# Kernel tuning notes

Hardware: AMD Instinct MI355X
Metric: run time of the kernel (lower is better)

Reference implementation:

```python
import jax, jax.numpy as jnp
import numpy as np

BSZ, SLEN, DIN = 4, 2048, 1024
EMB, HNO = 1024, 16
HSZ = EMB // HNO


def setup_inputs() -> dict:
    key = jax.random.key(0)
    ks = jax.random.split(key, 7)
    s = 1.0 / np.sqrt(DIN)
    return {
        "x": jax.random.normal(ks[0], (BSZ, SLEN, DIN), dtype=jnp.float32),
        "Wq": jax.random.uniform(ks[1], (EMB, DIN), jnp.float32, -s, s),
        "bq": jax.random.uniform(ks[2], (EMB,), jnp.float32, -s, s),
        "Wk": jax.random.uniform(ks[3], (EMB, DIN), jnp.float32, -s, s),
        "bk": jax.random.uniform(ks[4], (EMB,), jnp.float32, -s, s),
        "Wv": jax.random.uniform(ks[5], (EMB, DIN), jnp.float32, -s, s),
        "bv": jax.random.uniform(ks[6], (EMB,), jnp.float32, -s, s),
    }


def reference(x, Wq, bq, Wk, bk, Wv, bv):
    bsz, slen, _ = x.shape
    # QKV projections, split heads: [b, h, s, hd]
    def proj(W, b):
        y = jnp.einsum('bsd,ed->bse', x, W) + b
        return y.reshape(bsz, slen, HNO, HSZ).transpose(0, 2, 1, 3)
    q, k, v = proj(Wq, bq), proj(Wk, bk), proj(Wv, bv)
    # scaled causal attention scores [b, h, s, s]
    scores = jnp.einsum('bhqd,bhkd->bhqk', q, k) / jnp.sqrt(jnp.asarray(HSZ, x.dtype))
    causal = jnp.tril(jnp.ones((slen, slen), dtype=bool))
    scores = jnp.where(causal[None, None], scores, -jnp.inf)
    attn = jax.nn.softmax(scores, axis=-1)
    value = jnp.einsum('bhqk,bhkd->bhqd', attn, v)  # [b, h, s, hd]
    # faithful to source: swap (s, hd) THEN flatten to [b, s, emb]
    value = jnp.swapaxes(value, -2, -1).reshape(bsz, slen, -1)
    return value
```

## Files before the change

### kernel.cpp

```cpp
#include <hip/hip_runtime.h>


#define BSZ 4
#define SLEN 2048
#define DIN 1024
#define EMB 1024
#define HNO 16
#define HSZ 64

typedef unsigned short u16;
typedef __bf16 bf16x8_t __attribute__((ext_vector_type(8)));
typedef float f32x4_t __attribute__((ext_vector_type(4)));

__device__ __forceinline__ u16 f2bf(float f) {
    unsigned u = __float_as_uint(f);
    u += 0x7FFFu + ((u >> 16) & 1u);
    return (u16)(u >> 16);
}

__device__ __forceinline__ float exp2_fast(float x) {
    float r;
    asm("v_exp_f32 %0, %1" : "=v"(r) : "v"(x));
    return r;
}

__device__ __forceinline__ unsigned cvt_pk_bf16(float lo, float hi) {
    unsigned r;
    asm("v_cvt_pk_bf16_f32 %0, %1, %2" : "=v"(r) : "v"(lo), "v"(hi));
    return r;
}

__device__ __forceinline__ void gld16(void* lds, const void* g) {
    __builtin_amdgcn_global_load_lds(
        (const __attribute__((address_space(1))) void*)g,
        (__attribute__((address_space(3))) void*)lds, 16, 0, 0);
}

#define VMW0()                                                                 \
    do {                                                                       \
        asm volatile("s_waitcnt vmcnt(0)" ::: "memory");                       \
        __builtin_amdgcn_sched_barrier(0);                                     \
    } while (0)

#define LGKM0()                                                                \
    do {                                                                       \
        asm volatile("s_waitcnt lgkmcnt(0)" ::: "memory");                     \
        __builtin_amdgcn_sched_barrier(0);                                     \
    } while (0)

__global__ __launch_bounds__(256) void cvt_bf16_kernel(
    const float* __restrict__ x,  const float* __restrict__ wq,
    const float* __restrict__ wk, const float* __restrict__ wv,
    u16* __restrict__ xo, u16* __restrict__ wo)
{
    const int y = blockIdx.y;
    const float* src = (y == 0) ? x : (y == 1) ? wq : (y == 2) ? wk : wv;
    u16* dst = (y == 0) ? xo : wo + (size_t)(y - 1) * (EMB * DIN);
    const int n8 = (y == 0) ? (BSZ * SLEN * DIN / 8) : (EMB * DIN / 8);

    for (int i = blockIdx.x * 256 + threadIdx.x; i < n8; i += gridDim.x * 256) {
        float4 a = *reinterpret_cast<const float4*>(src + (size_t)i * 8);
        float4 b = *reinterpret_cast<const float4*>(src + (size_t)i * 8 + 4);
        union { u16 h[8]; uint4 u; } p;
        p.h[0] = f2bf(a.x); p.h[1] = f2bf(a.y); p.h[2] = f2bf(a.z); p.h[3] = f2bf(a.w);
        p.h[4] = f2bf(b.x); p.h[5] = f2bf(b.y); p.h[6] = f2bf(b.z); p.h[7] = f2bf(b.w);
        *reinterpret_cast<uint4*>(dst + (size_t)i * 8) = p.u;
    }
}

__global__ __launch_bounds__(256, 2) void qkv_gemm_kernel(
    const u16* __restrict__ xb, const u16* __restrict__ wb,
    const float* __restrict__ bq, const float* __restrict__ bk,
    const float* __restrict__ bv,
    u16* __restrict__ qkv, u16* __restrict__ vt)
{
    __shared__ __attribute__((aligned(16))) u16 SH[2 * 16384 + 8192];
    u16* Bs = SH + 2 * 16384;

    const int t    = threadIdx.x;
    const int wid  = t >> 6;
    const int lane = t & 63;
    const int g    = lane >> 4;
    const int r16  = lane & 15;
    const int wm   = wid >> 1, wn = wid & 1;

    const int wg  = blockIdx.x;
    const int xcd = wg & 7;
    const int j   = wg >> 3;
    const int jm  = j / 12;
    const int jn  = j - jm * 12;
    const int m0  = ((xcd & 3) * 8 + jm) * 256;
    const int n0g = ((xcd >> 2) * 12 + jn) * 128;

    const int rowoff = t >> 3;
    const int colswz = ((t & 7) ^ (rowoff & 7)) * 8;
    const u16* srcA = xb + (size_t)(m0 + rowoff) * DIN + colswz;
    const u16* srcB = wb + (size_t)(n0g + rowoff) * DIN + colswz;

    const int s0 = (g ^ (r16 & 7)) * 8;

    f32x4_t acc[8][4] = {};

#pragma unroll
    for (int u = 0; u < 8; ++u)
        gld16(SH + u * 2048 + t * 8, srcA + (size_t)u * 32 * DIN);
#pragma unroll
    for (int v = 0; v < 4; ++v)
        gld16(Bs + v * 2048 + t * 8, srcB + (size_t)v * 32 * DIN);
    VMW0();
    __builtin_amdgcn_s_barrier();

#pragma unroll 1
    for (int kt = 0; kt < 16; ++kt) {
        const bool nl = (kt != 15);
        const u16* Acur = SH + (kt & 1) * 16384;
        u16*       Aalt = SH + ((kt + 1) & 1) * 16384;

        if (nl) {
#pragma unroll
            for (int u = 0; u < 8; ++u)
                gld16(Aalt + u * 2048 + t * 8,
                      srcA + (size_t)u * 32 * DIN + (kt + 1) * 64);
        }

        bf16x8_t af[8], bf0[4], bf1[4];
#pragma unroll
        for (int i2 = 0; i2 < 8; ++i2)
            af[i2] = *reinterpret_cast<const bf16x8_t*>(
                Acur + (wm * 128 + i2 * 16 + r16) * 64 + s0);
#pragma unroll
        for (int j2 = 0; j2 < 4; ++j2) {
            bf0[j2] = *reinterpret_cast<const bf16x8_t*>(
                Bs + (wn * 64 + j2 * 16 + r16) * 64 + s0);
            bf1[j2] = *reinterpret_cast<const bf16x8_t*>(
                Bs + (wn * 64 + j2 * 16 + r16) * 64 + (s0 ^ 32));
        }

        __builtin_amdgcn_s_setprio(1);
#pragma unroll
        for (int i2 = 0; i2 < 8; ++i2)
#pragma unroll
            for (int j2 = 0; j2 < 4; ++j2)
                acc[i2][j2] = __builtin_amdgcn_mfma_f32_16x16x32_bf16(
                    af[i2], bf0[j2], acc[i2][j2], 0, 0, 0);
        __builtin_amdgcn_s_setprio(0);

#pragma unroll
        for (int i2 = 0; i2 < 8; ++i2)
            af[i2] = *reinterpret_cast<const bf16x8_t*>(
                Acur + (wm * 128 + i2 * 16 + r16) * 64 + (s0 ^ 32));

        LGKM0();
        __builtin_amdgcn_s_barrier();

        if (nl) {
#pragma unroll
            for (int v = 0; v < 4; ++v)
                gld16(Bs + v * 2048 + t * 8,
                      srcB + (size_t)v * 32 * DIN + (kt + 1) * 64);
        }

        __builtin_amdgcn_s_setprio(1);
#pragma unroll
        for (int i2 = 0; i2 < 8; ++i2)
#pragma unroll
            for (int j2 = 0; j2 < 4; ++j2)
                acc[i2][j2] = __builtin_amdgcn_mfma_f32_16x16x32_bf16(
                    af[i2], bf1[j2], acc[i2][j2], 0, 0, 0);
        __builtin_amdgcn_s_setprio(0);

        VMW0();
        __builtin_amdgcn_s_barrier();
    }

    const size_t per = (size_t)BSZ * HNO * SLEN * HSZ;
    const bool isV = (n0g >= 2 * 1024);
    u16* lout = SH;
    const int b  = m0 >> 11;
    const int sB = m0 & 2047;
    const int mat = n0g >> 10;

#pragma unroll
    for (int h = 0; h < 2; ++h) {
        __syncthreads();
        if (!isV) {
            if (wm == h) {
#pragma unroll
                for (int j2 = 0; j2 < 4; ++j2) {
                    const int el = wn * 64 + j2 * 16 + r16;
                    const int e  = (n0g + el) & 1023;
                    const float bval = (mat == 0) ? bq[e] : bk[e];
                    const float qsv  = (mat == 0) ? 0.125f * 1.44269504f : 1.0f;
#pragma unroll
                    for (int i2 = 0; i2 < 8; ++i2)
#pragma unroll
                        for (int r = 0; r < 4; ++r) {
                            int ml = i2 * 16 + g * 4 + r;
                            lout[ml * 136 + el] =
                                f2bf((acc[i2][j2][r] + bval) * qsv);
                        }
                }
            }
            __syncthreads();
#pragma unroll
            for (int it = 0; it < 8; ++it) {
                int cid = it * 256 + t;
                int row = cid >> 4;
                int cc  = cid & 15;
                int e   = (n0g + cc * 8) & 1023;
                int s   = sB + h * 128 + row;
                uint4 v = *reinterpret_cast<const uint4*>(&lout[row * 136 + cc * 8]);
                *reinterpret_cast<uint4*>(qkv + (size_t)mat * per +
                    ((((size_t)b * HNO) + (e >> 6)) * SLEN + s) * HSZ + (e & 63)) = v;
            }
        } else {
            if (wm == h) {
#pragma unroll
                for (int j2 = 0; j2 < 4; ++j2) {
                    const int el = wn * 64 + j2 * 16 + r16;
                    const int e  = (n0g + el) & 1023;
                    const float bval = bv[e];
#pragma unroll
                    for (int i2 = 0; i2 < 8; ++i2) {
                        uint2 pk;
                        pk.x = cvt_pk_bf16(acc[i2][j2][0] + bval,
                                           acc[i2][j2][1] + bval);
                        pk.y = cvt_pk_bf16(acc[i2][j2][2] + bval,
                                           acc[i2][j2][3] + bval);
                        *reinterpret_cast<uint2*>(
                            &lout[el * 136 + i2 * 16 + g * 4]) = pk;
                    }
                }
            }
            __syncthreads();
#pragma unroll
            for (int it = 0; it < 8; ++it) {
                int cid = it * 256 + t;
                int el  = cid >> 4;
                int sc  = cid & 15;
                int egl = n0g + el;
                int hh  = (egl >> 6) & 15;
                int d   = egl & 63;
                int s   = sB + h * 128 + sc * 8;
                uint4 v = *reinterpret_cast<const uint4*>(&lout[el * 136 + sc * 8]);
                *reinterpret_cast<uint4*>(vt +
                    (((size_t)(b * HNO + hh)) * HSZ + d) * SLEN + s) = v;
            }
        }
    }
}

__global__ __launch_bounds__(512, 6) void attn_kernel(
    const u16* __restrict__ qb, const u16* __restrict__ kb,
    const u16* __restrict__ vtg, float* __restrict__ out)
{
    __shared__ __attribute__((aligned(16))) u16 Ks[2][64][64];
    __shared__ __attribute__((aligned(16))) u16 Vt[2][64][64];
    __shared__ __attribute__((aligned(16))) u16 P2[8][16][72];

    const int t    = threadIdx.x;
    const int wid  = t >> 6;
    const int lane = t & 63;
    const int g    = lane >> 4;
    const int r16  = lane & 15;
    const int r8   = r16 & 7;

    const int w   = blockIdx.x;
    const int idx = w >> 3;
    const int bh  = (w & 7) * 8 + (idx & 7);
    const int qt  = 15 - (idx >> 3);
    const int q0  = qt * 128;
    const size_t base = (size_t)bh * (SLEN * HSZ);

    const int qi = q0 + wid * 16 + r16;
    bf16x8_t qf0 = *reinterpret_cast<const bf16x8_t*>(&qb[base + (size_t)qi * HSZ + g * 8]);
    bf16x8_t qf1 = *reinterpret_cast<const bf16x8_t*>(&qb[base + (size_t)qi * HSZ + 32 + g * 8]);

    const int srow = t >> 3;
    const int schk = ((t & 7) ^ (srow & 7)) * 8;
    const u16* ksrc = kb  + base + (size_t)srow * HSZ + schk;
    const u16* vsrc = vtg + base + (size_t)srow * SLEN + schk;
    const int ldst = wid * 8 * 64;

    f32x4_t o[4] = {};
    float lrow = 0.f;

    const int ntiles = 2 * qt + 2;
    const int qw0 = q0 + wid * 16;
    const int qmax_wave = qw0 + 15;

    gld16(&Ks[0][0][0] + ldst, ksrc);
    gld16(&Vt[0][0][0] + ldst, vsrc);
    VMW0();
    __builtin_amdgcn_s_barrier();

#pragma unroll 1
    for (int kt = 0; kt < ntiles; ++kt) {
        const int kv0  = kt * 64;
        const int bsel = kt & 1;
        if (kt + 1 < ntiles) {
            gld16(&Ks[bsel ^ 1][0][0] + ldst, ksrc + (size_t)(kv0 + 64) * HSZ);
            gld16(&Vt[bsel ^ 1][0][0] + ldst, vsrc + (kv0 + 64));
        }

        if (kv0 <= qmax_wave) {
            const u16* Kb = &Ks[bsel][0][0];
            const u16* Vb = &Vt[bsel][0][0];

            f32x4_t c_[4];
            __builtin_amdgcn_s_setprio(1);
#pragma unroll
            for (int m = 0; m < 4; ++m) {
                bf16x8_t a0 = *reinterpret_cast<const bf16x8_t*>(
                    Kb + (m * 16 + r16) * 64 + (g ^ r8) * 8);
                bf16x8_t a1 = *reinterpret_cast<const bf16x8_t*>(
                    Kb + (m * 16 + r16) * 64 + ((4 + g) ^ r8) * 8);
                f32x4_t cc = {};
                cc = __builtin_amdgcn_mfma_f32_16x16x32_bf16(a0, qf0, cc, 0, 0, 0);
                cc = __builtin_amdgcn_mfma_f32_16x16x32_bf16(a1, qf1, cc, 0, 0, 0);
                c_[m] = cc;
            }
            __builtin_amdgcn_s_setprio(0);

            float p[16];
            if (kv0 + 63 > qw0) {
#pragma unroll
                for (int m = 0; m < 4; ++m)
#pragma unroll
                    for (int r = 0; r < 4; ++r) {
                        int kj = kv0 + m * 16 + g * 4 + r;
                        float sv = (kj <= qi) ? c_[m][r] : -1e30f;
                        p[m * 4 + r] = exp2_fast(sv - 4.0f);
                    }
            } else {
#pragma unroll
                for (int m = 0; m < 4; ++m)
#pragma unroll
                    for (int r = 0; r < 4; ++r)
                        p[m * 4 + r] = exp2_fast(c_[m][r] - 4.0f);
            }
            float y0 = (p[0] + p[1]) + (p[2] + p[3]);
            float y1 = (p[4] + p[5]) + (p[6] + p[7]);
            float y2 = (p[8] + p[9]) + (p[10] + p[11]);
            float y3 = (p[12] + p[13]) + (p[14] + p[15]);
            float tsum = (y0 + y1) + (y2 + y3);
            tsum += __shfl_xor(tsum, 16);
            tsum += __shfl_xor(tsum, 32);
            lrow += tsum;

#pragma unroll
            for (int m = 0; m < 4; ++m) {
                uint2 pk;
                pk.x = cvt_pk_bf16(p[m * 4 + 0], p[m * 4 + 1]);
                pk.y = cvt_pk_bf16(p[m * 4 + 2], p[m * 4 + 3]);
                *reinterpret_cast<uint2*>(&P2[wid][r16][m * 16 + g * 4]) = pk;
            }

            __builtin_amdgcn_s_setprio(1);
#pragma unroll
            for (int c = 0; c < 2; ++c) {
                bf16x8_t pf = *reinterpret_cast<const bf16x8_t*>(
                    &P2[wid][r16][c * 32 + g * 8]);
#pragma unroll
                for (int j2 = 0; j2 < 4; ++j2) {
                    bf16x8_t vf = *reinterpret_cast<const bf16x8_t*>(
                        Vb + (j2 * 16 + r16) * 64 + ((c * 4 + g) ^ r8) * 8);
                    o[j2] = __builtin_amdgcn_mfma_f32_16x16x32_bf16(
                        vf, pf, o[j2], 0, 0, 0);
                }
            }
            __builtin_amdgcn_s_setprio(0);
        }

        VMW0();
        __builtin_amdgcn_s_barrier();
    }

    float rinv = 1.0f / lrow;
    const int b = bh >> 4, h = bh & 15;
    float* outb = out + (size_t)b * (SLEN * EMB) + (size_t)h * (HSZ * SLEN);
#pragma unroll
    for (int j2 = 0; j2 < 4; ++j2) {
#pragma unroll
        for (int r = 0; r < 4; ++r) {
            int d = j2 * 16 + g * 4 + r;
            outb[(size_t)d * SLEN + qi] = o[j2][r] * rinv;
        }
    }
}

extern "C" void kernel_launch(void* const* d_in, const int* in_sizes, int n_in,
                              void* d_out, int out_size, void* d_ws, size_t ws_size,
                              hipStream_t stream) {
    const float* x  = (const float*)d_in[0];
    const float* Wq = (const float*)d_in[1];
    const float* bq = (const float*)d_in[2];
    const float* Wk = (const float*)d_in[3];
    const float* bk = (const float*)d_in[4];
    const float* Wv = (const float*)d_in[5];
    const float* bv = (const float*)d_in[6];
    float* out = (float*)d_out;

    const size_t per = (size_t)BSZ * HNO * SLEN * HSZ;
    u16* qw = (u16*)d_ws;
    u16* kw = qw + per;
    u16* vw = kw + per;

    u16* xb = (u16*)d_out;
    u16* wb = xb + (size_t)BSZ * SLEN * DIN;

    cvt_bf16_kernel<<<dim3(256, 4), 256, 0, stream>>>(x, Wq, Wk, Wv, xb, wb);
    qkv_gemm_kernel<<<768, 256, 0, stream>>>(xb, wb, bq, bk, bv, qw, vw);
    attn_kernel<<<1024, 512, 0, stream>>>(qw, kw, vw, out);
}
```

Measured before the change: 122.2 us.

## Single-buffer A tile in QKV GEMM to shrink LDS and raise occupancy

Replaces the double-buffered A tile with one A buffer, cutting the GEMM's shared memory from about 80KB to 48KB. All next-tile global loads for A and B now issue after the second-half fragment reads and the barrier, and sched_barriers pin that ordering. The aim is lower LDS use, likely allowing more resident workgroups, and less register pressure from reusing one B fragment array. The cost is less overlap: the A prefetch no longer runs during the first half's MFMAs, so load latency is hidden only behind the second half.

```diff
diff --git a/kernel.cpp b/kernel.cpp
--- a/kernel.cpp
+++ b/kernel.cpp
@@ -74,8 +74,9 @@
     const float* __restrict__ bv,
     u16* __restrict__ qkv, u16* __restrict__ vt)
 {
-    __shared__ __attribute__((aligned(16))) u16 SH[2 * 16384 + 8192];
-    u16* Bs = SH + 2 * 16384;
+    __shared__ __attribute__((aligned(16))) u16 SH[256 * 64 + 128 * 64];
+    u16* AsF = SH;
+    u16* BsF = SH + 256 * 64;
 
     const int t    = threadIdx.x;
     const int wid  = t >> 6;
@@ -103,38 +104,25 @@
 
 #pragma unroll
     for (int u = 0; u < 8; ++u)
-        gld16(SH + u * 2048 + t * 8, srcA + (size_t)u * 32 * DIN);
+        gld16(AsF + u * 2048 + t * 8, srcA + (size_t)u * 32 * DIN);
 #pragma unroll
     for (int v = 0; v < 4; ++v)
-        gld16(Bs + v * 2048 + t * 8, srcB + (size_t)v * 32 * DIN);
+        gld16(BsF + v * 2048 + t * 8, srcB + (size_t)v * 32 * DIN);
     VMW0();
     __builtin_amdgcn_s_barrier();
 
 #pragma unroll 1
     for (int kt = 0; kt < 16; ++kt) {
-        const bool nl = (kt != 15);
-        const u16* Acur = SH + (kt & 1) * 16384;
-        u16*       Aalt = SH + ((kt + 1) & 1) * 16384;
-
-        if (nl) {
-#pragma unroll
-            for (int u = 0; u < 8; ++u)
-                gld16(Aalt + u * 2048 + t * 8,
-                      srcA + (size_t)u * 32 * DIN + (kt + 1) * 64);
-        }
-
-        bf16x8_t af[8], bf0[4], bf1[4];
+        bf16x8_t af[8], bf[4];
+
 #pragma unroll
         for (int i2 = 0; i2 < 8; ++i2)
             af[i2] = *reinterpret_cast<const bf16x8_t*>(
-                Acur + (wm * 128 + i2 * 16 + r16) * 64 + s0);
-#pragma unroll
-        for (int j2 = 0; j2 < 4; ++j2) {
-            bf0[j2] = *reinterpret_cast<const bf16x8_t*>(
-                Bs + (wn * 64 + j2 * 16 + r16) * 64 + s0);
-            bf1[j2] = *reinterpret_cast<const bf16x8_t*>(
-                Bs + (wn * 64 + j2 * 16 + r16) * 64 + (s0 ^ 32));
-        }
+                AsF + (wm * 128 + i2 * 16 + r16) * 64 + s0);
+#pragma unroll
+        for (int j2 = 0; j2 < 4; ++j2)
+            bf[j2] = *reinterpret_cast<const bf16x8_t*>(
+                BsF + (wn * 64 + j2 * 16 + r16) * 64 + s0);
 
         __builtin_amdgcn_s_setprio(1);
 #pragma unroll
@@ -142,23 +130,33 @@
 #pragma unroll
             for (int j2 = 0; j2 < 4; ++j2)
                 acc[i2][j2] = __builtin_amdgcn_mfma_f32_16x16x32_bf16(
-                    af[i2], bf0[j2], acc[i2][j2], 0, 0, 0);
+                    af[i2], bf[j2], acc[i2][j2], 0, 0, 0);
         __builtin_amdgcn_s_setprio(0);
 
 #pragma unroll
         for (int i2 = 0; i2 < 8; ++i2)
             af[i2] = *reinterpret_cast<const bf16x8_t*>(
-                Acur + (wm * 128 + i2 * 16 + r16) * 64 + (s0 ^ 32));
+                AsF + (wm * 128 + i2 * 16 + r16) * 64 + (s0 ^ 32));
+#pragma unroll
+        for (int j2 = 0; j2 < 4; ++j2)
+            bf[j2] = *reinterpret_cast<const bf16x8_t*>(
+                BsF + (wn * 64 + j2 * 16 + r16) * 64 + (s0 ^ 32));
 
         LGKM0();
         __builtin_amdgcn_s_barrier();
-
-        if (nl) {
+        __builtin_amdgcn_sched_barrier(0);
+
+        if (kt != 15) {
+#pragma unroll
+            for (int u = 0; u < 8; ++u)
+                gld16(AsF + u * 2048 + t * 8,
+                      srcA + (size_t)u * 32 * DIN + (kt + 1) * 64);
 #pragma unroll
             for (int v = 0; v < 4; ++v)
-                gld16(Bs + v * 2048 + t * 8,
+                gld16(BsF + v * 2048 + t * 8,
                       srcB + (size_t)v * 32 * DIN + (kt + 1) * 64);
         }
+        __builtin_amdgcn_sched_barrier(0);
 
         __builtin_amdgcn_s_setprio(1);
 #pragma unroll
@@ -166,8 +164,9 @@
 #pragma unroll
             for (int j2 = 0; j2 < 4; ++j2)
                 acc[i2][j2] = __builtin_amdgcn_mfma_f32_16x16x32_bf16(
-                    af[i2], bf1[j2], acc[i2][j2], 0, 0, 0);
+                    af[i2], bf[j2], acc[i2][j2], 0, 0, 0);
         __builtin_amdgcn_s_setprio(0);
+        __builtin_amdgcn_sched_barrier(0);
 
         VMW0();
         __builtin_amdgcn_s_barrier();
```

After: 125.0 us. 1.02x slower.
